# Optimization experiments

Hardware: AMD Instinct MI355X
Metric: run time of the kernel (lower is better)

The kernel has to match this reference:

```python
import jax, jax.numpy as jnp
import numpy as np

N = 1_000_000
G = 64          # grid_size (square)
F = 32          # feature_dim
K = 3           # num_components
TWO_PI = 2.0 * np.pi


def _linear_init(key, out_dim, in_dim):
    # kaiming-uniform-ish scale, exact init does not matter for correctness baseline
    bound = 1.0 / np.sqrt(in_dim)
    return jax.random.uniform(key, (out_dim, in_dim), minval=-bound, maxval=bound, dtype=jnp.float32)


def setup_inputs() -> dict:
    key = jax.random.key(0)
    ks = jax.random.split(key, 10)
    coords = jax.random.uniform(ks[0], (N, 3), minval=-1.0, maxval=1.0, dtype=jnp.float32)
    feature_grid = jax.random.normal(ks[1], (G, G, F), dtype=jnp.float32)
    # xy_net: Linear(2+F,128) ReLU Linear(128,64) ReLU
    W1 = _linear_init(ks[2], 128, 2 + F); b1 = jnp.zeros((128,), jnp.float32)
    W2 = _linear_init(ks[3], 64, 128);    b2 = jnp.zeros((64,), jnp.float32)
    # SIREN: SineLayer(1,128, w0=30, first) -> SineLayer(128,64, w0=1)
    Ws1 = jax.random.uniform(ks[4], (128, 1), minval=-1.0, maxval=1.0, dtype=jnp.float32)
    bs1 = jnp.zeros((128,), jnp.float32)
    c = np.sqrt(6.0 / 128.0) / 1.0
    Ws2 = jax.random.uniform(ks[5], (64, 128), minval=-c, maxval=c, dtype=jnp.float32)
    bs2 = jnp.zeros((64,), jnp.float32)
    # FiLM: Linear(64, 128) + Tanh
    Wf = _linear_init(ks[6], 128, 64); bf = jnp.zeros((128,), jnp.float32)
    # head: Linear(64, 6*K), structured bias init
    Wh = _linear_init(ks[7], 6 * K, 64)
    bh = np.zeros((K, 6), np.float32)
    bh[:, 1] = 0.1
    bh[:, 3] = -1.386
    bh[:, 4] = -1.386
    bh = jnp.asarray(bh.reshape(-1))
    return dict(coords=coords, feature_grid=feature_grid,
                W1=W1, b1=b1, W2=W2, b2=b2,
                Ws1=Ws1, bs1=bs1, Ws2=Ws2, bs2=bs2,
                Wf=Wf, bf=bf, Wh=Wh, bh=bh)


def reference(coords, feature_grid, W1, b1, W2, b2, Ws1, bs1, Ws2, bs2, Wf, bf, Wh, bh):
    Gy, Gx, _ = feature_grid.shape
    # --- bilinear gather from feature grid ---
    x_idx = (coords[:, 0] + 1.0) * 0.5 * (Gx - 1)
    y_idx = (coords[:, 1] + 1.0) * 0.5 * (Gy - 1)
    x0 = jnp.clip(jnp.floor(x_idx).astype(jnp.int32), 0, Gx - 2)
    y0 = jnp.clip(jnp.floor(y_idx).astype(jnp.int32), 0, Gy - 2)
    x1 = x0 + 1
    y1 = y0 + 1
    dx = (x_idx - x0.astype(jnp.float32))[:, None]   # [N,1]
    dy = (y_idx - y0.astype(jnp.float32))[:, None]
    f00 = feature_grid[y0, x0]   # [N,F]
    f01 = feature_grid[y1, x0]
    f10 = feature_grid[y0, x1]
    f11 = feature_grid[y1, x1]
    spat = ((1 - dx) * (1 - dy) * f00 + (1 - dx) * dy * f01
            + dx * (1 - dy) * f10 + dx * dy * f11)
    # --- xy MLP ---
    xy_in = jnp.concatenate([coords[:, 0:2], spat], axis=-1)            # [N,2+F]
    h = jax.nn.relu(xy_in @ W1.T + b1)
    h_xy = jax.nn.relu(h @ W2.T + b2)                                    # [N,64]
    # --- SIREN on t ---
    t = coords[:, 2:3]
    ht = jnp.sin(30.0 * (t @ Ws1.T + bs1))                               # omega_0_first
    h_t = jnp.sin(1.0 * (ht @ Ws2.T + bs2))                              # omega_0_hidden [N,64]
    # --- FiLM fusion ---
    gamma_beta = jnp.tanh(h_t @ Wf.T + bf)                               # [N,128]
    Hxy = h_xy.shape[-1]
    gamma = 1.0 + 0.1 * gamma_beta[:, :Hxy]
    beta = gamma_beta[:, Hxy:]
    fused = gamma * h_xy + beta                                          # [N,64]
    # --- head + GMM param postproc ---
    params = (fused @ Wh.T + bh).reshape(-1, K, 6)                       # [N,K,6]
    weights = jax.nn.softmax(params[:, :, 0], axis=-1)
    speed = jax.nn.relu(params[:, :, 1])
    angle = jnp.mod(params[:, :, 2], TWO_PI)
    variances = jnp.exp(jnp.clip(params[:, :, 3:5], -10.0, 10.0))
    corr = 0.99 * jnp.tanh(params[:, :, 5])
    gmm = jnp.concatenate([weights[..., None],
                           jnp.stack([speed, angle], axis=-1),
                           variances,
                           corr[..., None]], axis=-1)                    # [N,K,6]
    return (gmm, coords)
```

## Files before the change

kernel.cpp:

```cpp
#include <hip/hip_runtime.h>
#include <math.h>

#define NPTS 1000000
#define NWORDS 31250
#define NKEYS 262144
#define LIST_CAP 262144
#define TWO_PI_D 6.283185307179586
#define TWO_PI_F 6.28318530717958647692f

#define OFF_W1   0
#define OFF_W1T  4352
#define OFF_W2T  8704
#define OFF_WS1  16896
#define OFF_BS1  17024
#define OFF_WS2T 17152
#define OFF_BS2  25344
#define OFF_WFT  25408
#define OFF_BF   33600
#define OFF_WHT  33728
#define OFF_BH   34880
#define OFF_B1   34898
#define OFF_B2   35026
#define WD_DOUBLES 35090

#define W2T32_OFF  280832
#define PROJ_OFF   313600
#define BMP_OFF    2410752
#define CNT_OFF    2536192
#define GB_OFF     2541824
#define HIST_OFF   4638976
#define PART_OFF   5687552
#define W1XY_OFF   5691648
#define BFH_OFF    5692672
#define BFL_OFF    5709056
#define CSORT_OFF  5725440
#define WS_SORT_MIN (CSORT_OFF + 16000000ull)

typedef __attribute__((ext_vector_type(8))) short bf16x8;
typedef __attribute__((ext_vector_type(4))) float f32x4;

__device__ __forceinline__ short f2bf(float x) {
    unsigned u = __float_as_uint(x);
    unsigned r = (u + 0x7FFFu + ((u >> 16) & 1u)) >> 16;
    return (short)r;
}
__device__ __forceinline__ float bf2f(short s) {
    return __uint_as_float(((unsigned)(unsigned short)s) << 16);
}
__device__ __forceinline__ void st4(float* d, float4 v) {
    d[0] = v.x; d[1] = v.y; d[2] = v.z; d[3] = v.w;
}

__global__ __launch_bounds__(256) void prep_k(
    const float* __restrict__ W1, const float* __restrict__ b1,
    const float* __restrict__ W2, const float* __restrict__ b2,
    const float* __restrict__ Ws1, const float* __restrict__ bs1,
    const float* __restrict__ Ws2, const float* __restrict__ bs2,
    const float* __restrict__ Wf, const float* __restrict__ bf,
    const float* __restrict__ Wh, const float* __restrict__ bh,
    char* __restrict__ ws)
{
    double* wd = (double*)ws;
    float* w2t32 = (float*)(ws + W2T32_OFF);
    float2* w1xyp = (float2*)(ws + W1XY_OFF);
    short* bfh = (short*)(ws + BFH_OFF);
    short* bfl = (short*)(ws + BFL_OFF);
    int i = blockIdx.x * 256 + threadIdx.x;
    if (i < 4352) {
        wd[OFF_W1 + i] = (double)W1[i];
        int row = i >> 7, col = i & 127;
        wd[OFF_W1T + i] = (double)W1[col * 34 + row];
    }
    if (i < 8192) {
        int j = i >> 6, k = i & 63;
        float w2v = W2[k * 128 + j];
        wd[OFF_W2T + i] = (double)w2v;  w2t32[i] = w2v;
        wd[OFF_WS2T + i] = (double)Ws2[k * 128 + j];
        int m = i >> 7, r = i & 127;
        wd[OFF_WFT + i] = (double)Wf[r * 64 + m];
    }
    if (i < 8192) {
        int jj = i & 7, l = (i >> 3) & 63, f = i >> 9;
        int ks = f >> 2, nt = f & 3;
        int j = ks * 32 + ((l >> 4) << 3) + jj;
        int nn = nt * 16 + (l & 15);
        float v = W2[nn * 128 + j];
        short hi = f2bf(v);
        bfh[i] = hi;
        bfl[i] = f2bf(v - bf2f(hi));
    }
    if (i < 1152) {
        int m = i % 18, k = i / 18;
        wd[OFF_WHT + i] = (double)Wh[m * 64 + k];
    }
    if (i < 128) {
        wd[OFF_WS1 + i] = (double)Ws1[i];
        wd[OFF_BS1 + i] = (double)bs1[i];
        wd[OFF_BF  + i] = (double)bf[i];
        wd[OFF_B1  + i] = (double)b1[i];
        w1xyp[i] = make_float2(W1[i * 34], W1[i * 34 + 1]);
    }
    if (i < 64) {
        wd[OFF_BS2 + i] = (double)bs2[i];
        wd[OFF_B2  + i] = (double)b2[i];
    }
    if (i < 18) wd[OFF_BH + i] = (double)bh[i];
}

__global__ __launch_bounds__(256) void build_proj(
    const float* __restrict__ grid, const double* __restrict__ wd,
    float* __restrict__ proj, unsigned* __restrict__ bmp,
    unsigned* __restrict__ hist, unsigned* __restrict__ cnt)
{
    int idx = blockIdx.x * 256 + threadIdx.x;
    if (idx < NWORDS) bmp[idx] = 0u;
    if (hist && idx < NKEYS) hist[idx] = 0u;
    if (idx == 0) *cnt = 0u;
    if (idx >= 64 * 64 * 128) return;
    int j = idx & 127, node = idx >> 7;
    const double* W1T = wd + OFF_W1T;
    const float* g = grid + node * 32;
    double s0 = 0, s1 = 0, s2 = 0, s3 = 0;
#pragma unroll
    for (int i = 0; i < 32; i += 4) {
        s0 = fma((double)g[i + 0], W1T[(2 + i + 0) * 128 + j], s0);
        s1 = fma((double)g[i + 1], W1T[(2 + i + 1) * 128 + j], s1);
        s2 = fma((double)g[i + 2], W1T[(2 + i + 2) * 128 + j], s2);
        s3 = fma((double)g[i + 3], W1T[(2 + i + 3) * 128 + j], s3);
    }
    proj[idx] = (float)((s0 + s2) + (s1 + s3));
}

__global__ __launch_bounds__(256) void build_gb(
    const double* __restrict__ wd, float* __restrict__ GB, int bins)
{
    __shared__ double sh[4 * 128];
    int wid = threadIdx.x >> 6, lane = threadIdx.x & 63;
    double* buf = sh + wid * 128;
    int bin = blockIdx.x * 4 + wid;
    if (bin >= bins) return;
    double t = -1.0 + 2.0 * (double)bin / (double)(bins - 1);

    buf[lane]      = sin(30.0 * fma(t, wd[OFF_WS1 + lane],      wd[OFF_BS1 + lane]));
    buf[lane + 64] = sin(30.0 * fma(t, wd[OFF_WS1 + 64 + lane], wd[OFF_BS1 + 64 + lane]));
    __threadfence_block();
    double a0 = wd[OFF_BS2 + lane], a1 = 0, a2 = 0, a3 = 0;
    const double* W = wd + OFF_WS2T;
#pragma unroll 2
    for (int j = 0; j < 128; j += 4) {
        a0 = fma(buf[j + 0], W[(j + 0) * 64 + lane], a0);
        a1 = fma(buf[j + 1], W[(j + 1) * 64 + lane], a1);
        a2 = fma(buf[j + 2], W[(j + 2) * 64 + lane], a2);
        a3 = fma(buf[j + 3], W[(j + 3) * 64 + lane], a3);
    }
    double ht = sin((a0 + a2) + (a1 + a3));
    __threadfence_block();
    buf[lane] = ht;
    __threadfence_block();
    double g0 = wd[OFF_BF + lane], g1 = 0, e0 = wd[OFF_BF + 64 + lane], e1 = 0;
    const double* WT = wd + OFF_WFT;
#pragma unroll 2
    for (int m = 0; m < 64; m += 2) {
        double h0 = buf[m], h1 = buf[m + 1];
        g0 = fma(h0, WT[(m + 0) * 128 + lane], g0);
        g1 = fma(h1, WT[(m + 1) * 128 + lane], g1);
        e0 = fma(h0, WT[(m + 0) * 128 + 64 + lane], e0);
        e1 = fma(h1, WT[(m + 1) * 128 + 64 + lane], e1);
    }
    GB[(size_t)bin * 128 + lane]      = (float)fma(0.1, tanh(g0 + g1), 1.0);
    GB[(size_t)bin * 128 + 64 + lane] = (float)tanh(e0 + e1);
}

__device__ __forceinline__ unsigned point_key(float xf, float yf, float tf)
{
    float xi = (xf + 1.0f) * 0.5f * 63.0f;
    float yi = (yf + 1.0f) * 0.5f * 63.0f;
    int x0 = (int)floorf(xi); x0 = x0 < 0 ? 0 : (x0 > 62 ? 62 : x0);
    int y0 = (int)floorf(yi); y0 = y0 < 0 ? 0 : (y0 > 62 ? 62 : y0);
    float u = (tf + 1.0f) * 32.0f;
    int tb = (int)u; tb = tb < 0 ? 0 : (tb > 63 ? 63 : tb);
    return ((unsigned)(y0 * 64 + x0) << 6) | (unsigned)tb;
}

__global__ __launch_bounds__(256) void hist_k(
    const float* __restrict__ coords, unsigned* __restrict__ hist)
{
    int n = blockIdx.x * 256 + threadIdx.x;
    if (n >= NPTS) return;
    unsigned key = point_key(coords[3 * n], coords[3 * n + 1], coords[3 * n + 2]);
    atomicAdd(&hist[key], 1u);
}

__global__ __launch_bounds__(256) void scan1_k(
    const unsigned* __restrict__ hist, unsigned* __restrict__ part)
{
    __shared__ unsigned s[256];
    int t = threadIdx.x;
    s[t] = hist[blockIdx.x * 256 + t];
    __syncthreads();
    for (int off = 128; off > 0; off >>= 1) {
        if (t < off) s[t] += s[t + off];
        __syncthreads();
    }
    if (t == 0) part[blockIdx.x] = s[0];
}

__global__ __launch_bounds__(1024) void scan2_k(unsigned* __restrict__ part)
{
    __shared__ unsigned s[1024];
    int t = threadIdx.x;
    unsigned orig = part[t];
    s[t] = orig;
    __syncthreads();
    for (int off = 1; off < 1024; off <<= 1) {
        unsigned tmp = (t >= off) ? s[t - off] : 0u;
        __syncthreads();
        s[t] += tmp;
        __syncthreads();
    }
    part[t] = s[t] - orig;
}

__global__ __launch_bounds__(256) void scan3_k(
    unsigned* __restrict__ hist, const unsigned* __restrict__ part)
{
    __shared__ unsigned s[256];
    int t = threadIdx.x;
    int i = blockIdx.x * 256 + t;
    unsigned orig = hist[i];
    s[t] = orig;
    __syncthreads();
    for (int off = 1; off < 256; off <<= 1) {
        unsigned tmp = (t >= off) ? s[t - off] : 0u;
        __syncthreads();
        s[t] += tmp;
        __syncthreads();
    }
    hist[i] = s[t] - orig + part[blockIdx.x];
}

__global__ __launch_bounds__(256) void scatter_k(
    const float* __restrict__ coords, unsigned* __restrict__ offs,
    float4* __restrict__ csort)
{
    int n = blockIdx.x * 256 + threadIdx.x;
    if (n >= NPTS) return;
    float xf = coords[3 * n], yf = coords[3 * n + 1], tf = coords[3 * n + 2];
    unsigned key = point_key(xf, yf, tf);
    unsigned pos = atomicAdd(&offs[key], 1u);
    csort[pos] = make_float4(xf, yf, tf, __int_as_float(n));
}

__device__ __forceinline__ void eval_pt_wave(
    int n, int lane, double* buf,
    const float* __restrict__ coords, const float* __restrict__ grid,
    const double* __restrict__ wd, float* __restrict__ out, bool wrc)
{
    const float xf = coords[3 * n + 0];
    const float yf = coords[3 * n + 1];
    const float tf = coords[3 * n + 2];

    double xi = ((double)xf + 1.0) * 0.5 * 63.0;
    double yi = ((double)yf + 1.0) * 0.5 * 63.0;
    int x0 = (int)floor(xi); x0 = x0 < 0 ? 0 : (x0 > 62 ? 62 : x0);
    int y0 = (int)floor(yi); y0 = y0 < 0 ? 0 : (y0 > 62 ? 62 : y0);
    double dx = xi - (double)x0;
    double dy = yi - (double)y0;
    double w00 = (1.0 - dx) * (1.0 - dy);
    double w01 = (1.0 - dx) * dy;
    double w10 = dx * (1.0 - dy);
    double w11 = dx * dy;
    const float* f00 = grid + ((size_t)(y0 * 64 + x0)) * 32;

    if (lane < 32) {
        double v = (w00 * (double)f00[lane] + w01 * (double)f00[2048 + lane])
                 + (w10 * (double)f00[32 + lane] + w11 * (double)f00[2080 + lane]);
        buf[192 + 2 + lane] = v;
    } else if (lane == 32) buf[192 + 0] = (double)xf;
    else if (lane == 33)   buf[192 + 1] = (double)yf;
    __threadfence_block();

    double hlo = wd[OFF_B1 + lane], hhi = wd[OFF_B1 + 64 + lane];
    {
        const double* W = wd + OFF_W1T;
#pragma unroll 2
        for (int i = 0; i < 34; ++i) {
            double xv = buf[192 + i];
            hlo = fma(xv, W[i * 128 + lane], hlo);
            hhi = fma(xv, W[i * 128 + 64 + lane], hhi);
        }
    }
    buf[lane]      = fmax(hlo, 0.0);
    buf[64 + lane] = fmax(hhi, 0.0);
    __threadfence_block();

    double c0 = wd[OFF_B2 + lane], c1 = 0, c2 = 0, c3 = 0;
    {
        const double* W = wd + OFF_W2T;
#pragma unroll 2
        for (int j = 0; j < 128; j += 4) {
            c0 = fma(buf[j + 0], W[(j + 0) * 64 + lane], c0);
            c1 = fma(buf[j + 1], W[(j + 1) * 64 + lane], c1);
            c2 = fma(buf[j + 2], W[(j + 2) * 64 + lane], c2);
            c3 = fma(buf[j + 3], W[(j + 3) * 64 + lane], c3);
        }
    }
    double hxy = fmax((c0 + c2) + (c1 + c3), 0.0);
    __threadfence_block();

    double tt = (double)tf;
    buf[lane]      = sin(30.0 * fma(tt, wd[OFF_WS1 + lane],      wd[OFF_BS1 + lane]));
    buf[64 + lane] = sin(30.0 * fma(tt, wd[OFF_WS1 + 64 + lane], wd[OFF_BS1 + 64 + lane]));
    __threadfence_block();
    double a0 = wd[OFF_BS2 + lane], a1 = 0, a2 = 0, a3 = 0;
    {
        const double* W = wd + OFF_WS2T;
#pragma unroll 2
        for (int j = 0; j < 128; j += 4) {
            a0 = fma(buf[j + 0], W[(j + 0) * 64 + lane], a0);
            a1 = fma(buf[j + 1], W[(j + 1) * 64 + lane], a1);
            a2 = fma(buf[j + 2], W[(j + 2) * 64 + lane], a2);
            a3 = fma(buf[j + 3], W[(j + 3) * 64 + lane], a3);
        }
    }
    buf[128 + lane] = sin((a0 + a2) + (a1 + a3));
    __threadfence_block();

    double g0 = wd[OFF_BF + lane], g1 = 0, e0 = wd[OFF_BF + 64 + lane], e1 = 0;
    {
        const double* W = wd + OFF_WFT;
#pragma unroll 2
        for (int m = 0; m < 64; m += 2) {
            double h0 = buf[128 + m], h1 = buf[128 + m + 1];
            g0 = fma(h0, W[(m + 0) * 128 + lane], g0);
            g1 = fma(h1, W[(m + 1) * 128 + lane], g1);
            e0 = fma(h0, W[(m + 0) * 128 + 64 + lane], e0);
            e1 = fma(h1, W[(m + 1) * 128 + 64 + lane], e1);
        }
    }
    double fused = fma(fma(0.1, tanh(g0 + g1), 1.0), hxy, tanh(e0 + e1));
    __threadfence_block();
    buf[lane] = fused;
    __threadfence_block();

    if (lane < 18) {
        const double* W = wd + OFF_WHT;
        double p0 = wd[OFF_BH + lane], p1 = 0;
#pragma unroll 2
        for (int k = 0; k < 64; k += 2) {
            p0 = fma(buf[k + 0], W[(k + 0) * 18 + lane], p0);
            p1 = fma(buf[k + 1], W[(k + 1) * 18 + lane], p1);
        }
        buf[128 + lane] = p0 + p1;
    }
    __threadfence_block();

    if (lane < 18) {
        int m6 = lane % 6;
        double p = buf[128 + lane];
        float ov;
        if (m6 == 0) {
            double l0 = buf[128 + 0], l1 = buf[128 + 6], l2 = buf[128 + 12];
            double mx = fmax(l0, fmax(l1, l2));
            double s = exp(l0 - mx) + exp(l1 - mx) + exp(l2 - mx);
            ov = (float)(exp(p - mx) / s);
        } else if (m6 == 1) ov = (float)fmax(p, 0.0);
        else if (m6 == 2)   ov = (float)(p - floor(p / TWO_PI_D) * TWO_PI_D);
        else if (m6 == 5)   ov = (float)(0.99 * tanh(p));
        else { double v = fmin(fmax(p, -10.0), 10.0); ov = (float)exp(v); }
        out[(size_t)n * 18 + lane] = ov;
    }
    if (wrc && lane < 3)
        out[(size_t)18 * NPTS + (size_t)n * 3 + lane] = coords[3 * n + lane];
    __threadfence_block();
}

__device__ __forceinline__ void eval_angle_wave(
    int n, int lane, double* buf,
    const float* __restrict__ coords, const float* __restrict__ grid,
    const double* __restrict__ wd, const float* __restrict__ Wh,
    const float* __restrict__ bh, float* __restrict__ out)
{
    const float xf = coords[3 * n + 0];
    const float yf = coords[3 * n + 1];
    const float tf = coords[3 * n + 2];

    double xi = ((double)xf + 1.0) * 0.5 * 63.0;
    double yi = ((double)yf + 1.0) * 0.5 * 63.0;
    int x0 = (int)floor(xi); x0 = x0 < 0 ? 0 : (x0 > 62 ? 62 : x0);
    int y0 = (int)floor(yi); y0 = y0 < 0 ? 0 : (y0 > 62 ? 62 : y0);
    double dx = xi - (double)x0;
    double dy = yi - (double)y0;
    double w00 = (1.0 - dx) * (1.0 - dy);
    double w01 = (1.0 - dx) * dy;
    double w10 = dx * (1.0 - dy);
    double w11 = dx * dy;
    const float* f00 = grid + ((size_t)(y0 * 64 + x0)) * 32;

    if (lane < 32) {
        double v = (w00 * (double)f00[lane] + w01 * (double)f00[2048 + lane])
                 + (w10 * (double)f00[32 + lane] + w11 * (double)f00[2080 + lane]);
        buf[192 + 2 + lane] = v;
    } else if (lane == 32) buf[192 + 0] = (double)xf;
    else if (lane == 33)   buf[192 + 1] = (double)yf;
    __threadfence_block();

    double hlo = wd[OFF_B1 + lane], hhi = wd[OFF_B1 + 64 + lane];
    {
        const double* W = wd + OFF_W1T;
#pragma unroll 2
        for (int i = 0; i < 34; ++i) {
            double xv = buf[192 + i];
            hlo = fma(xv, W[i * 128 + lane], hlo);
            hhi = fma(xv, W[i * 128 + 64 + lane], hhi);
        }
    }
    buf[lane]      = fmax(hlo, 0.0);
    buf[64 + lane] = fmax(hhi, 0.0);
    __threadfence_block();

    double c0 = wd[OFF_B2 + lane], c1 = 0, c2 = 0, c3 = 0;
    {
        const double* W = wd + OFF_W2T;
#pragma unroll 2
        for (int j = 0; j < 128; j += 4) {
            c0 = fma(buf[j + 0], W[(j + 0) * 64 + lane], c0);
            c1 = fma(buf[j + 1], W[(j + 1) * 64 + lane], c1);
            c2 = fma(buf[j + 2], W[(j + 2) * 64 + lane], c2);
            c3 = fma(buf[j + 3], W[(j + 3) * 64 + lane], c3);
        }
    }
    double hxy = fmax((c0 + c2) + (c1 + c3), 0.0);
    __threadfence_block();

    double tt = (double)tf;
    buf[lane]      = sin(30.0 * fma(tt, wd[OFF_WS1 + lane],      wd[OFF_BS1 + lane]));
    buf[64 + lane] = sin(30.0 * fma(tt, wd[OFF_WS1 + 64 + lane], wd[OFF_BS1 + 64 + lane]));
    __threadfence_block();
    double a0 = wd[OFF_BS2 + lane], a1 = 0, a2 = 0, a3 = 0;
    {
        const double* W = wd + OFF_WS2T;
#pragma unroll 2
        for (int j = 0; j < 128; j += 4) {
            a0 = fma(buf[j + 0], W[(j + 0) * 64 + lane], a0);
            a1 = fma(buf[j + 1], W[(j + 1) * 64 + lane], a1);
            a2 = fma(buf[j + 2], W[(j + 2) * 64 + lane], a2);
            a3 = fma(buf[j + 3], W[(j + 3) * 64 + lane], a3);
        }
    }
    buf[128 + lane] = sin((a0 + a2) + (a1 + a3));
    __threadfence_block();

    double g0 = wd[OFF_BF + lane], g1 = 0, e0 = wd[OFF_BF + 64 + lane], e1 = 0;
    {
        const double* W = wd + OFF_WFT;
#pragma unroll 2
        for (int m = 0; m < 64; m += 2) {
            double h0 = buf[128 + m], h1 = buf[128 + m + 1];
            g0 = fma(h0, W[(m + 0) * 128 + lane], g0);
            g1 = fma(h1, W[(m + 1) * 128 + lane], g1);
            e0 = fma(h0, W[(m + 0) * 128 + 64 + lane], e0);
            e1 = fma(h1, W[(m + 1) * 128 + 64 + lane], e1);
        }
    }
    double fused = fma(fma(0.1, tanh(g0 + g1), 1.0), hxy, tanh(e0 + e1));

    double p2  = fused * (double)Wh[2 * 64 + lane];
    double p8  = fused * (double)Wh[8 * 64 + lane];
    double p14 = fused * (double)Wh[14 * 64 + lane];
#pragma unroll
    for (int off = 32; off > 0; off >>= 1) {
        p2  += __shfl_xor(p2, off);
        p8  += __shfl_xor(p8, off);
        p14 += __shfl_xor(p14, off);
    }
    if (lane == 0) {
        double q2  = p2  + (double)bh[2];
        double q8  = p8  + (double)bh[8];
        double q14 = p14 + (double)bh[14];
        out[(size_t)n * 18 + 2]  = (float)(q2  - floor(q2  / TWO_PI_D) * TWO_PI_D);
        out[(size_t)n * 18 + 8]  = (float)(q8  - floor(q8  / TWO_PI_D) * TWO_PI_D);
        out[(size_t)n * 18 + 14] = (float)(q14 - floor(q14 / TWO_PI_D) * TWO_PI_D);
    }
    __threadfence_block();
}

__global__ __launch_bounds__(64) void repair_list(
    const float* __restrict__ coords, const float* __restrict__ grid,
    const double* __restrict__ wd, const float* __restrict__ Wh,
    const float* __restrict__ bh, const unsigned* __restrict__ cnt,
    const unsigned* __restrict__ list, float* __restrict__ out)
{
    __shared__ double buf[232];
    int lane = threadIdx.x;
    unsigned total = *cnt;
    if (total > LIST_CAP) total = LIST_CAP;
    for (unsigned i = blockIdx.x; i < total; i += gridDim.x)
        eval_angle_wave((int)list[i], lane, buf, coords, grid, wd, Wh, bh, out);
}

__global__ __launch_bounds__(64) void repair_bmp(
    const float* __restrict__ coords, const float* __restrict__ grid,
    const double* __restrict__ wd, const unsigned* __restrict__ bmp,
    float* __restrict__ out)
{
    __shared__ double buf[232];
    int lane = threadIdx.x;
    for (unsigned w = blockIdx.x; w < NWORDS; w += gridDim.x) {
        unsigned word = bmp[w];
        while (word) {
            unsigned b = (unsigned)__builtin_ctz(word);
            word &= word - 1;
            eval_pt_wave((int)(w * 32 + b), lane, buf, coords, grid, wd, out, false);
        }
    }
}

__global__ __launch_bounds__(64) void full_f64_fb(
    const float* __restrict__ coords, const float* __restrict__ grid,
    const double* __restrict__ wd, float* __restrict__ out)
{
    __shared__ double buf[232];
    int lane = threadIdx.x;
    for (unsigned n = blockIdx.x; n < NPTS; n += gridDim.x)
        eval_pt_wave((int)n, lane, buf, coords, grid, wd, out, true);
}

__global__ __launch_bounds__(64) void main_mfma(
    const float4* __restrict__ csort,
    const float* __restrict__ proj, const float* __restrict__ GB,
    const short* __restrict__ bfH, const short* __restrict__ bfL,
    const float* __restrict__ w1xy, const float* __restrict__ b1,
    const float* __restrict__ b2,
    const float* __restrict__ Wh, const float* __restrict__ bh,
    int bins, float tau, float* __restrict__ out,
    unsigned* __restrict__ cnt, unsigned* __restrict__ list,
    unsigned* __restrict__ bmp)
{
    __shared__ float wl[2048];
    const int lane = threadIdx.x;
    const int wavebase = blockIdx.x * 64;

    f32x4 acc[4][4];
#pragma unroll
    for (int a = 0; a < 4; ++a)
#pragma unroll
        for (int b = 0; b < 4; ++b) acc[a][b] = (f32x4){0.f, 0.f, 0.f, 0.f};

    float4 myc = csort[wavebase + lane];
    float w00, w01, w10, w11; int node;
    {
        float xi = (myc.x + 1.0f) * 0.5f * 63.0f;
        float yi = (myc.y + 1.0f) * 0.5f * 63.0f;
        int x0 = (int)floorf(xi); x0 = x0 < 0 ? 0 : (x0 > 62 ? 62 : x0);
        int y0 = (int)floorf(yi); y0 = y0 < 0 ? 0 : (y0 > 62 ? 62 : y0);
        float dx = xi - (float)x0;
        float dy = yi - (float)y0;
        w00 = (1.0f - dx) * (1.0f - dy);
        w01 = (1.0f - dx) * dy;
        w10 = dx * (1.0f - dy);
        w11 = dx * dy;
        node = y0 * 64 + x0;
    }
    float px[4], py[4], pw00[4], pw01[4], pw10[4], pw11[4];
    int pnode[4];
#pragma unroll
    for (int mt = 0; mt < 4; ++mt) {
        int src = mt * 16 + (lane & 15);
        px[mt]   = __shfl(myc.x, src);
        py[mt]   = __shfl(myc.y, src);
        pw00[mt] = __shfl(w00, src);
        pw01[mt] = __shfl(w01, src);
        pw10[mt] = __shfl(w10, src);
        pw11[mt] = __shfl(w11, src);
        pnode[mt] = __shfl(node, src);
    }

#pragma unroll 2
    for (int ks = 0; ks < 4; ++ks) {
        const int dbase = ks * 32 + ((lane >> 4) << 3);
        bf16x8 bHf[4], bLf[4];
#pragma unroll
        for (int nt = 0; nt < 4; ++nt) {
            int fi = ((ks * 4 + nt) * 64 + lane) * 8;
            bHf[nt] = *(const bf16x8*)(bfH + fi);
            bLf[nt] = *(const bf16x8*)(bfL + fi);
        }
        float b1r[8];
        st4(b1r,     *(const float4*)(b1 + dbase));
        st4(b1r + 4, *(const float4*)(b1 + dbase + 4));
        float wvr[16];
        {
            const float4* wxy = (const float4*)w1xy + (dbase >> 1);
            st4(wvr,      wxy[0]);
            st4(wvr + 4,  wxy[1]);
            st4(wvr + 8,  wxy[2]);
            st4(wvr + 12, wxy[3]);
        }
#pragma unroll
        for (int mt = 0; mt < 4; ++mt) {
            const float* pj = proj + pnode[mt] * 128 + dbase;
            float q00[8], q10[8], q01[8], q11[8];
            st4(q00,     *(const float4*)(pj));
            st4(q00 + 4, *(const float4*)(pj + 4));
            st4(q10,     *(const float4*)(pj + 128));
            st4(q10 + 4, *(const float4*)(pj + 132));
            st4(q01,     *(const float4*)(pj + 8192));
            st4(q01 + 4, *(const float4*)(pj + 8196));
            st4(q11,     *(const float4*)(pj + 8320));
            st4(q11 + 4, *(const float4*)(pj + 8324));
            bf16x8 ah, al;
            float xx = px[mt], yy = py[mt];
            float a00 = pw00[mt], a01 = pw01[mt], a10 = pw10[mt], a11 = pw11[mt];
#pragma unroll
            for (int jj = 0; jj < 8; ++jj) {
                float h = b1r[jj];
                h = fmaf(xx, wvr[jj * 2], h);
                h = fmaf(yy, wvr[jj * 2 + 1], h);
                h = fmaf(a00, q00[jj], h);
                h = fmaf(a01, q01[jj], h);
                h = fmaf(a10, q10[jj], h);
                h = fmaf(a11, q11[jj], h);
                h = fmaxf(h, 0.0f);
                short hi = f2bf(h);
                ah[jj] = hi;
                al[jj] = f2bf(h - bf2f(hi));
            }
#pragma unroll
            for (int nt = 0; nt < 4; ++nt) {
                acc[mt][nt] = __builtin_amdgcn_mfma_f32_16x16x32_bf16(ah, bHf[nt], acc[mt][nt], 0, 0, 0);
                acc[mt][nt] = __builtin_amdgcn_mfma_f32_16x16x32_bf16(ah, bLf[nt], acc[mt][nt], 0, 0, 0);
                acc[mt][nt] = __builtin_amdgcn_mfma_f32_16x16x32_bf16(al, bHf[nt], acc[mt][nt], 0, 0, 0);
            }
        }
    }

    float pp[18];
    int ib, n_out;
    float ft;
    {
        float u = (myc.z + 1.0f) * 0.5f * (float)(bins - 1);
        ib = (int)u; ib = ib < 0 ? 0 : (ib > bins - 2 ? bins - 2 : ib);
        ft = u - (float)ib;
        n_out = __float_as_int(myc.w);
#pragma unroll
        for (int m = 0; m < 18; ++m) pp[m] = bh[m];
    }
    const int rbase = ((lane >> 4) << 2);
#pragma unroll
    for (int half = 0; half < 2; ++half) {
#pragma unroll
        for (int nt2 = 0; nt2 < 2; ++nt2) {
            int nt = half * 2 + nt2;
            int kl = nt2 * 16 + (lane & 15);
#pragma unroll
            for (int mt = 0; mt < 4; ++mt)
#pragma unroll
                for (int r = 0; r < 4; ++r) {
                    int pt = mt * 16 + rbase + r;
                    wl[kl * 64 + ((pt + kl) & 63)] = acc[mt][nt][r];
                }
        }
        __syncthreads();
        {
            const float* GAg = GB + (size_t)ib * 128 + half * 32;
            const float* GAe = GAg + 64;
            const float* GBg = GB + (size_t)(ib + 1) * 128 + half * 32;
            const float* GBe = GBg + 64;
#pragma unroll
            for (int c = 0; c < 8; ++c) {
                float g0r[4], g1r[4], e0r[4], e1r[4];
                st4(g0r, *(const float4*)(GAg + c * 4));
                st4(g1r, *(const float4*)(GBg + c * 4));
                st4(e0r, *(const float4*)(GAe + c * 4));
                st4(e1r, *(const float4*)(GBe + c * 4));
#pragma unroll
                for (int q = 0; q < 4; ++q) {
                    int kl = c * 4 + q, k = half * 32 + kl;
                    float v = wl[kl * 64 + ((lane + kl) & 63)];
                    float a = fmaxf(v + b2[k], 0.0f);
                    float ga = fmaf(ft, g1r[q] - g0r[q], g0r[q]);
                    float be = fmaf(ft, e1r[q] - e0r[q], e0r[q]);
                    float fz = fmaf(ga, a, be);
#pragma unroll
                    for (int m = 0; m < 18; ++m)
                        pp[m] = fmaf(fz, Wh[m * 64 + k], pp[m]);
                }
            }
        }
        __syncthreads();
    }

    float o[18];
    bool flag = false;
    {
        float l0 = pp[0], l1 = pp[6], l2 = pp[12];
        float mx = fmaxf(l0, fmaxf(l1, l2));
        float ex0 = __expf(l0 - mx), ex1 = __expf(l1 - mx), ex2 = __expf(l2 - mx);
        float inv = __fdividef(1.0f, ex0 + ex1 + ex2);
        o[0] = ex0 * inv; o[6] = ex1 * inv; o[12] = ex2 * inv;
#pragma unroll
        for (int kk = 0; kk < 3; ++kk) {
            o[kk * 6 + 1] = fmaxf(pp[kk * 6 + 1], 0.0f);
            float an = pp[kk * 6 + 2];
            float fl = floorf(an * (1.0f / TWO_PI_F));
            o[kk * 6 + 2] = an - fl * TWO_PI_F;
            float r = an - TWO_PI_F * rintf(an * (1.0f / TWO_PI_F));
            if (fabsf(r) < tau) flag = true;
            float v1 = fminf(fmaxf(pp[kk * 6 + 3], -10.0f), 10.0f);
            o[kk * 6 + 3] = __expf(v1);
            float v2 = fminf(fmaxf(pp[kk * 6 + 4], -10.0f), 10.0f);
            o[kk * 6 + 4] = __expf(v2);
            float e2 = __expf(2.0f * pp[kk * 6 + 5]);
            o[kk * 6 + 5] = 0.99f * __fdividef(e2 - 1.0f, e2 + 1.0f);
        }
    }

    float* og = out + (size_t)n_out * 18;
#pragma unroll
    for (int i = 0; i < 18; i += 2)
        *reinterpret_cast<float2*>(og + i) = make_float2(o[i], o[i + 1]);
    float* oc = out + (size_t)18 * NPTS + (size_t)n_out * 3;
    oc[0] = myc.x; oc[1] = myc.y; oc[2] = myc.z;

    if (flag) {
        unsigned idx = atomicAdd(cnt, 1u);
        if (idx < LIST_CAP) list[idx] = (unsigned)n_out;
        else atomicOr(&bmp[n_out >> 5], 1u << (n_out & 31));
    }
}

__global__ __launch_bounds__(256) void main_unsorted(
    const float* __restrict__ coords,
    const float* __restrict__ W1, const float* __restrict__ b1,
    const float* __restrict__ b2,
    const float* __restrict__ Wh, const float* __restrict__ bh,
    const float* __restrict__ W2T,
    const float* __restrict__ PROJ, const float* __restrict__ GB,
    int bins, float tau,
    float* __restrict__ out, unsigned* __restrict__ bmp)
{
    int n = blockIdx.x * 256 + threadIdx.x;
    if (n >= NPTS) return;
    float xf = coords[3 * n], yf = coords[3 * n + 1], tf = coords[3 * n + 2];

    float xi = (xf + 1.0f) * 0.5f * 63.0f;
    float yi = (yf + 1.0f) * 0.5f * 63.0f;
    int x0 = (int)floorf(xi); x0 = x0 < 0 ? 0 : (x0 > 62 ? 62 : x0);
    int y0 = (int)floorf(yi); y0 = y0 < 0 ? 0 : (y0 > 62 ? 62 : y0);
    float dx = xi - (float)x0;
    float dy = yi - (float)y0;
    float w00 = (1.0f - dx) * (1.0f - dy);
    float w01 = (1.0f - dx) * dy;
    float w10 = dx * (1.0f - dy);
    float w11 = dx * dy;
    int node = y0 * 64 + x0;

    float u = (tf + 1.0f) * 0.5f * (float)(bins - 1);
    int ib = (int)u; ib = ib < 0 ? 0 : (ib > bins - 2 ? bins - 2 : ib);
    float ft = u - (float)ib;

    const float4* P00 = (const float4*)(PROJ + (size_t)node * 128);
    const float4* P10 = P00 + 32;
    const float4* P01 = P00 + 2048;
    const float4* P11 = P01 + 32;

    float acc[64];
#pragma unroll
    for (int k = 0; k < 64; ++k) acc[k] = b2[k];

#pragma unroll 1
    for (int jb = 0; jb < 32; ++jb) {
        float4 a00 = P00[jb], a01 = P01[jb], a10 = P10[jb], a11 = P11[jb];
        const float* a00f = (const float*)&a00;
        const float* a01f = (const float*)&a01;
        const float* a10f = (const float*)&a10;
        const float* a11f = (const float*)&a11;
        const float* w1b = W1 + jb * 136;
#pragma unroll
        for (int q = 0; q < 4; ++q) {
            float hq = b1[jb * 4 + q];
            hq = fmaf(xf, w1b[q * 34 + 0], hq);
            hq = fmaf(yf, w1b[q * 34 + 1], hq);
            hq = fmaf(w00, a00f[q], hq);
            hq = fmaf(w01, a01f[q], hq);
            hq = fmaf(w10, a10f[q], hq);
            hq = fmaf(w11, a11f[q], hq);
            hq = fmaxf(hq, 0.0f);
            const float* w2c = W2T + (jb * 4 + q) * 64;
#pragma unroll
            for (int k = 0; k < 64; ++k) acc[k] = fmaf(hq, w2c[k], acc[k]);
        }
    }
#pragma unroll
    for (int k = 0; k < 64; ++k) acc[k] = fmaxf(acc[k], 0.0f);

    float pp[18];
#pragma unroll
    for (int m = 0; m < 18; ++m) pp[m] = bh[m];

    const float4* GA = (const float4*)(GB + (size_t)ib * 128);
    const float4* GBn = (const float4*)(GB + (size_t)(ib + 1) * 128);
#pragma unroll
    for (int kb = 0; kb < 16; ++kb) {
        float4 g0 = GA[kb], g1 = GBn[kb], e0 = GA[16 + kb], e1 = GBn[16 + kb];
        const float* g0f = (const float*)&g0;
        const float* g1f = (const float*)&g1;
        const float* e0f = (const float*)&e0;
        const float* e1f = (const float*)&e1;
        float fz[4];
#pragma unroll
        for (int q = 0; q < 4; ++q) {
            float ga = fmaf(ft, g1f[q] - g0f[q], g0f[q]);
            float be = fmaf(ft, e1f[q] - e0f[q], e0f[q]);
            fz[q] = fmaf(ga, acc[kb * 4 + q], be);
        }
#pragma unroll
        for (int m = 0; m < 18; ++m) {
            const float* whr = Wh + m * 64 + kb * 4;
            float pm = pp[m];
            pm = fmaf(fz[0], whr[0], pm);
            pm = fmaf(fz[1], whr[1], pm);
            pm = fmaf(fz[2], whr[2], pm);
            pm = fmaf(fz[3], whr[3], pm);
            pp[m] = pm;
        }
    }

    float o[18];
    bool flag = false;
    {
        float l0 = pp[0], l1 = pp[6], l2 = pp[12];
        float mx = fmaxf(l0, fmaxf(l1, l2));
        float ex0 = __expf(l0 - mx), ex1 = __expf(l1 - mx), ex2 = __expf(l2 - mx);
        float inv = __fdividef(1.0f, ex0 + ex1 + ex2);
        o[0] = ex0 * inv; o[6] = ex1 * inv; o[12] = ex2 * inv;
#pragma unroll
        for (int kk = 0; kk < 3; ++kk) {
            o[kk * 6 + 1] = fmaxf(pp[kk * 6 + 1], 0.0f);
            float an = pp[kk * 6 + 2];
            float fl = floorf(an * (1.0f / TWO_PI_F));
            o[kk * 6 + 2] = an - fl * TWO_PI_F;
            float r = an - TWO_PI_F * rintf(an * (1.0f / TWO_PI_F));
            if (fabsf(r) < tau) flag = true;
            float v1 = fminf(fmaxf(pp[kk * 6 + 3], -10.0f), 10.0f);
            o[kk * 6 + 3] = __expf(v1);
            float v2 = fminf(fmaxf(pp[kk * 6 + 4], -10.0f), 10.0f);
            o[kk * 6 + 4] = __expf(v2);
            float e2 = __expf(2.0f * pp[kk * 6 + 5]);
            o[kk * 6 + 5] = 0.99f * __fdividef(e2 - 1.0f, e2 + 1.0f);
        }
    }

    float* og = out + (size_t)n * 18;
#pragma unroll
    for (int i = 0; i < 18; i += 2)
        *reinterpret_cast<float2*>(og + i) = make_float2(o[i], o[i + 1]);
    float* oc = out + (size_t)18 * NPTS + (size_t)n * 3;
    oc[0] = xf; oc[1] = yf; oc[2] = tf;

    if (flag) atomicOr(&bmp[n >> 5], 1u << (n & 31));
}

extern "C" void kernel_launch(void* const* d_in, const int* in_sizes, int n_in,
                              void* d_out, int out_size, void* d_ws, size_t ws_size,
                              hipStream_t stream) {
    const float* coords = (const float*)d_in[0];
    const float* grid   = (const float*)d_in[1];
    const float* W1  = (const float*)d_in[2];
    const float* b1  = (const float*)d_in[3];
    const float* W2  = (const float*)d_in[4];
    const float* b2  = (const float*)d_in[5];
    const float* Ws1 = (const float*)d_in[6];
    const float* bs1 = (const float*)d_in[7];
    const float* Ws2 = (const float*)d_in[8];
    const float* bs2 = (const float*)d_in[9];
    const float* Wf  = (const float*)d_in[10];
    const float* bf  = (const float*)d_in[11];
    const float* Wh  = (const float*)d_in[12];
    const float* bh  = (const float*)d_in[13];
    char* ws = (char*)d_ws;
    double* wd = (double*)ws;
    float* out = (float*)d_out;

    prep_k<<<32, 256, 0, stream>>>(W1, b1, W2, b2, Ws1, bs1, Ws2, bs2,
                                   Wf, bf, Wh, bh, ws);

    size_t need1024 = (size_t)GB_OFF + 1024ull * 512ull;
    size_t need4096 = (size_t)GB_OFF + 4096ull * 512ull;
    if (ws_size < need1024) {
        full_f64_fb<<<16384, 64, 0, stream>>>(coords, grid, wd, out);
        return;
    }

    float* W2T32 = (float*)(ws + W2T32_OFF);
    float* proj  = (float*)(ws + PROJ_OFF);
    unsigned* bmp = (unsigned*)(ws + BMP_OFF);
    unsigned* cnt = (unsigned*)(ws + CNT_OFF);
    float* gbt   = (float*)(ws + GB_OFF);

    const int nblk = (NPTS + 255) / 256;
    if (ws_size >= WS_SORT_MIN) {
        int bins = 4096; float tau = 5.0e-4f;
        unsigned* hist = (unsigned*)(ws + HIST_OFF);
        unsigned* part = (unsigned*)(ws + PART_OFF);
        float* w1xyp   = (float*)(ws + W1XY_OFF);
        short* bfh     = (short*)(ws + BFH_OFF);
        short* bfl     = (short*)(ws + BFL_OFF);
        float4* csort  = (float4*)(ws + CSORT_OFF);

        build_proj<<<2048, 256, 0, stream>>>(grid, wd, proj, bmp, hist, cnt);
        build_gb<<<1024, 256, 0, stream>>>(wd, gbt, bins);
        hist_k<<<nblk, 256, 0, stream>>>(coords, hist);
        scan1_k<<<NKEYS / 256, 256, 0, stream>>>(hist, part);
        scan2_k<<<1, 1024, 0, stream>>>(part);
        scan3_k<<<NKEYS / 256, 256, 0, stream>>>(hist, part);
        scatter_k<<<nblk, 256, 0, stream>>>(coords, hist, csort);
        main_mfma<<<NPTS / 64, 64, 0, stream>>>(
            csort, proj, gbt, bfh, bfl, w1xyp, b1, b2, Wh, bh,
            bins, tau, out, cnt, hist , bmp);
        repair_list<<<8192, 64, 0, stream>>>(coords, grid, wd, Wh, bh,
                                             cnt, hist, out);
        repair_bmp<<<2048, 64, 0, stream>>>(coords, grid, wd, bmp, out);
    } else {
        int bins = (ws_size >= need4096) ? 4096 : 1024;
        float tau = (bins >= 4096) ? 1.5e-3f : 5.0e-3f;
        build_proj<<<2048, 256, 0, stream>>>(grid, wd, proj, bmp,
                                             (unsigned*)nullptr, cnt);
        build_gb<<<(bins + 3) / 4, 256, 0, stream>>>(wd, gbt, bins);
        main_unsorted<<<nblk, 256, 0, stream>>>(
            coords, W1, b1, b2, Wh, bh, W2T32, proj, gbt, bins, tau, out, bmp);
        repair_bmp<<<2048, 64, 0, stream>>>(coords, grid, wd, bmp, out);
    }
}
```

Measured before the change: 561.0 us.

## Fuse projection, GB table and histogram setup into one launch

Merges build_proj, build_gb and hist_k into a single block-partitioned setup kernel, and moves the bitmap, counter and histogram zeroing into prep_k. This cuts kernel launches and the gaps between dependent launches in the sorted path. Also changes the main_mfma ks loop from unroll 2 to unroll 1, likely to reduce register pressure, and halves the repair_list grid. The histogram atomics now run alongside the proj and GB work inside one grid.

```diff
diff --git a/kernel.cpp b/kernel.cpp
--- a/kernel.cpp
+++ b/kernel.cpp
@@ -36,6 +36,11 @@
 #define CSORT_OFF  5725440
 #define WS_SORT_MIN (CSORT_OFF + 16000000ull)
 
+#define SB_PROJ 2048
+#define SB_GB   1024
+#define SB_HIST 3907
+#define SETUP_BLKS (SB_PROJ + SB_GB + SB_HIST)
+
 typedef __attribute__((ext_vector_type(8))) short bf16x8;
 typedef __attribute__((ext_vector_type(4))) float f32x4;
 
@@ -49,6 +54,17 @@
 }
 __device__ __forceinline__ void st4(float* d, float4 v) {
     d[0] = v.x; d[1] = v.y; d[2] = v.z; d[3] = v.w;
+}
+
+__device__ __forceinline__ unsigned point_key(float xf, float yf, float tf)
+{
+    float xi = (xf + 1.0f) * 0.5f * 63.0f;
+    float yi = (yf + 1.0f) * 0.5f * 63.0f;
+    int x0 = (int)floorf(xi); x0 = x0 < 0 ? 0 : (x0 > 62 ? 62 : x0);
+    int y0 = (int)floorf(yi); y0 = y0 < 0 ? 0 : (y0 > 62 ? 62 : y0);
+    float u = (tf + 1.0f) * 32.0f;
+    int tb = (int)u; tb = tb < 0 ? 0 : (tb > 63 ? 63 : tb);
+    return ((unsigned)(y0 * 64 + x0) << 6) | (unsigned)tb;
 }
 
 __global__ __launch_bounds__(256) void prep_k(
@@ -58,7 +74,7 @@
     const float* __restrict__ Ws2, const float* __restrict__ bs2,
     const float* __restrict__ Wf, const float* __restrict__ bf,
     const float* __restrict__ Wh, const float* __restrict__ bh,
-    char* __restrict__ ws)
+    char* __restrict__ ws, int zmode)
 {
     double* wd = (double*)ws;
     float* w2t32 = (float*)(ws + W2T32_OFF);
@@ -66,6 +82,17 @@
     short* bfh = (short*)(ws + BFH_OFF);
     short* bfl = (short*)(ws + BFL_OFF);
     int i = blockIdx.x * 256 + threadIdx.x;
+
+    if (zmode >= 1) {
+        unsigned* bmp = (unsigned*)(ws + BMP_OFF);
+        for (int j = i; j < NWORDS; j += 32 * 256) bmp[j] = 0u;
+        if (i == 0) *(unsigned*)(ws + CNT_OFF) = 0u;
+    }
+    if (zmode >= 2) {
+        unsigned* hist = (unsigned*)(ws + HIST_OFF);
+        for (int j = i; j < NKEYS; j += 32 * 256) hist[j] = 0u;
+    }
+
     if (i < 4352) {
         wd[OFF_W1 + i] = (double)W1[i];
         int row = i >> 7, col = i & 127;
@@ -107,15 +134,77 @@
     if (i < 18) wd[OFF_BH + i] = (double)bh[i];
 }
 
+__global__ __launch_bounds__(256) void setup_k(
+    const float* __restrict__ grid, const double* __restrict__ wd,
+    float* __restrict__ proj, float* __restrict__ GB,
+    const float* __restrict__ coords, unsigned* __restrict__ hist)
+{
+    __shared__ double sh[4 * 128];
+    const int b = blockIdx.x;
+
+    if (b < SB_PROJ) {
+        int idx = b * 256 + threadIdx.x;
+        int j = idx & 127, node = idx >> 7;
+        const double* W1T = wd + OFF_W1T;
+        const float* g = grid + node * 32;
+        double s0 = 0, s1 = 0, s2 = 0, s3 = 0;
+#pragma unroll
+        for (int i = 0; i < 32; i += 4) {
+            s0 = fma((double)g[i + 0], W1T[(2 + i + 0) * 128 + j], s0);
+            s1 = fma((double)g[i + 1], W1T[(2 + i + 1) * 128 + j], s1);
+            s2 = fma((double)g[i + 2], W1T[(2 + i + 2) * 128 + j], s2);
+            s3 = fma((double)g[i + 3], W1T[(2 + i + 3) * 128 + j], s3);
+        }
+        proj[idx] = (float)((s0 + s2) + (s1 + s3));
+    } else if (b < SB_PROJ + SB_GB) {
+        int wid = threadIdx.x >> 6, lane = threadIdx.x & 63;
+        double* buf = sh + wid * 128;
+        int bin = (b - SB_PROJ) * 4 + wid;
+        double t = -1.0 + 2.0 * (double)bin / 4095.0;
+
+        buf[lane]      = sin(30.0 * fma(t, wd[OFF_WS1 + lane],      wd[OFF_BS1 + lane]));
+        buf[lane + 64] = sin(30.0 * fma(t, wd[OFF_WS1 + 64 + lane], wd[OFF_BS1 + 64 + lane]));
+        __threadfence_block();
+        double a0 = wd[OFF_BS2 + lane], a1 = 0, a2 = 0, a3 = 0;
+        const double* W = wd + OFF_WS2T;
+#pragma unroll 2
+        for (int j = 0; j < 128; j += 4) {
+            a0 = fma(buf[j + 0], W[(j + 0) * 64 + lane], a0);
+            a1 = fma(buf[j + 1], W[(j + 1) * 64 + lane], a1);
+            a2 = fma(buf[j + 2], W[(j + 2) * 64 + lane], a2);
+            a3 = fma(buf[j + 3], W[(j + 3) * 64 + lane], a3);
+        }
+        double ht = sin((a0 + a2) + (a1 + a3));
+        __threadfence_block();
+        buf[lane] = ht;
+        __threadfence_block();
+        double g0 = wd[OFF_BF + lane], g1 = 0, e0 = wd[OFF_BF + 64 + lane], e1 = 0;
+        const double* WT = wd + OFF_WFT;
+#pragma unroll 2
+        for (int m = 0; m < 64; m += 2) {
+            double h0 = buf[m], h1 = buf[m + 1];
+            g0 = fma(h0, WT[(m + 0) * 128 + lane], g0);
+            g1 = fma(h1, WT[(m + 1) * 128 + lane], g1);
+            e0 = fma(h0, WT[(m + 0) * 128 + 64 + lane], e0);
+            e1 = fma(h1, WT[(m + 1) * 128 + 64 + lane], e1);
+        }
+        GB[(size_t)bin * 128 + lane]      = (float)fma(0.1, tanh(g0 + g1), 1.0);
+        GB[(size_t)bin * 128 + 64 + lane] = (float)tanh(e0 + e1);
+    } else {
+        int n = (b - SB_PROJ - SB_GB) * 256 + threadIdx.x;
+        if (n < NPTS) {
+            unsigned key = point_key(coords[3 * n], coords[3 * n + 1],
+                                     coords[3 * n + 2]);
+            atomicAdd(&hist[key], 1u);
+        }
+    }
+}
+
 __global__ __launch_bounds__(256) void build_proj(
     const float* __restrict__ grid, const double* __restrict__ wd,
-    float* __restrict__ proj, unsigned* __restrict__ bmp,
-    unsigned* __restrict__ hist, unsigned* __restrict__ cnt)
+    float* __restrict__ proj)
 {
     int idx = blockIdx.x * 256 + threadIdx.x;
-    if (idx < NWORDS) bmp[idx] = 0u;
-    if (hist && idx < NKEYS) hist[idx] = 0u;
-    if (idx == 0) *cnt = 0u;
     if (idx >= 64 * 64 * 128) return;
     int j = idx & 127, node = idx >> 7;
     const double* W1T = wd + OFF_W1T;
@@ -169,26 +258,6 @@
     }
     GB[(size_t)bin * 128 + lane]      = (float)fma(0.1, tanh(g0 + g1), 1.0);
     GB[(size_t)bin * 128 + 64 + lane] = (float)tanh(e0 + e1);
-}
-
-__device__ __forceinline__ unsigned point_key(float xf, float yf, float tf)
-{
-    float xi = (xf + 1.0f) * 0.5f * 63.0f;
-    float yi = (yf + 1.0f) * 0.5f * 63.0f;
-    int x0 = (int)floorf(xi); x0 = x0 < 0 ? 0 : (x0 > 62 ? 62 : x0);
-    int y0 = (int)floorf(yi); y0 = y0 < 0 ? 0 : (y0 > 62 ? 62 : y0);
-    float u = (tf + 1.0f) * 32.0f;
-    int tb = (int)u; tb = tb < 0 ? 0 : (tb > 63 ? 63 : tb);
-    return ((unsigned)(y0 * 64 + x0) << 6) | (unsigned)tb;
-}
-
-__global__ __launch_bounds__(256) void hist_k(
-    const float* __restrict__ coords, unsigned* __restrict__ hist)
-{
-    int n = blockIdx.x * 256 + threadIdx.x;
-    if (n >= NPTS) return;
-    unsigned key = point_key(coords[3 * n], coords[3 * n + 1], coords[3 * n + 2]);
-    atomicAdd(&hist[key], 1u);
 }
 
 __global__ __launch_bounds__(256) void scan1_k(
@@ -576,7 +645,7 @@
         pnode[mt] = __shfl(node, src);
     }
 
-#pragma unroll 2
+#pragma unroll 1
     for (int ks = 0; ks < 4; ++ks) {
         const int dbase = ks * 32 + ((lane >> 4) << 3);
         bf16x8 bHf[4], bLf[4];
@@ -883,12 +952,12 @@
     double* wd = (double*)ws;
     float* out = (float*)d_out;
 
-    prep_k<<<32, 256, 0, stream>>>(W1, b1, W2, b2, Ws1, bs1, Ws2, bs2,
-                                   Wf, bf, Wh, bh, ws);
-
     size_t need1024 = (size_t)GB_OFF + 1024ull * 512ull;
     size_t need4096 = (size_t)GB_OFF + 4096ull * 512ull;
+
     if (ws_size < need1024) {
+        prep_k<<<32, 256, 0, stream>>>(W1, b1, W2, b2, Ws1, bs1, Ws2, bs2,
+                                       Wf, bf, Wh, bh, ws, 0);
         full_f64_fb<<<16384, 64, 0, stream>>>(coords, grid, wd, out);
         return;
     }
@@ -909,9 +978,10 @@
         short* bfl     = (short*)(ws + BFL_OFF);
         float4* csort  = (float4*)(ws + CSORT_OFF);
 
-        build_proj<<<2048, 256, 0, stream>>>(grid, wd, proj, bmp, hist, cnt);
-        build_gb<<<1024, 256, 0, stream>>>(wd, gbt, bins);
-        hist_k<<<nblk, 256, 0, stream>>>(coords, hist);
+        prep_k<<<32, 256, 0, stream>>>(W1, b1, W2, b2, Ws1, bs1, Ws2, bs2,
+                                       Wf, bf, Wh, bh, ws, 2);
+        setup_k<<<SETUP_BLKS, 256, 0, stream>>>(grid, wd, proj, gbt,
+                                                coords, hist);
         scan1_k<<<NKEYS / 256, 256, 0, stream>>>(hist, part);
         scan2_k<<<1, 1024, 0, stream>>>(part);
         scan3_k<<<NKEYS / 256, 256, 0, stream>>>(hist, part);
@@ -919,14 +989,15 @@
         main_mfma<<<NPTS / 64, 64, 0, stream>>>(
             csort, proj, gbt, bfh, bfl, w1xyp, b1, b2, Wh, bh,
             bins, tau, out, cnt, hist , bmp);
-        repair_list<<<8192, 64, 0, stream>>>(coords, grid, wd, Wh, bh,
+        repair_list<<<4096, 64, 0, stream>>>(coords, grid, wd, Wh, bh,
                                              cnt, hist, out);
         repair_bmp<<<2048, 64, 0, stream>>>(coords, grid, wd, bmp, out);
     } else {
         int bins = (ws_size >= need4096) ? 4096 : 1024;
         float tau = (bins >= 4096) ? 1.5e-3f : 5.0e-3f;
-        build_proj<<<2048, 256, 0, stream>>>(grid, wd, proj, bmp,
-                                             (unsigned*)nullptr, cnt);
+        prep_k<<<32, 256, 0, stream>>>(W1, b1, W2, b2, Ws1, bs1, Ws2, bs2,
+                                       Wf, bf, Wh, bh, ws, 1);
+        build_proj<<<2048, 256, 0, stream>>>(grid, wd, proj);
         build_gb<<<(bins + 3) / 4, 256, 0, stream>>>(wd, gbt, bins);
         main_unsorted<<<nblk, 256, 0, stream>>>(
             coords, W1, b1, b2, Wh, bh, W2T32, proj, gbt, bins, tau, out, bmp);
```

New measurement: 544.7 us. 2.9% less time.
